# Kernel tuning notes

Measured on AMD Instinct MI355X. Metric: run time of the kernel, lower is better.

Reference implementation:

```python
import jax, jax.numpy as jnp
import numpy as np

QMIN, QMAX = -128.0, 127.0  # int8 range

def setup_inputs() -> dict:
    key = jax.random.key(0)
    k1, k2 = jax.random.split(key)
    B, S, D_IN, D_OUT = 4, 2048, 4096, 4096
    x = jax.random.normal(k1, (B, S, D_IN), dtype=jnp.float32)
    # int8 weight stored as int32 (values in int8 range)
    weight = jax.random.randint(k2, (D_OUT, D_IN), -128, 128, dtype=jnp.int32)
    scale = jnp.array([0.02], dtype=jnp.float32)        # per-tensor weight scale
    input_scale = jnp.array([0.05], dtype=jnp.float32)  # static activation scale
    return {"x": x, "weight": weight, "scale": scale, "input_scale": input_scale}

def reference(x, weight, scale, input_scale):
    # quantize_static_quant_activations: round(x/input_scale) clamped to int8 range,
    # then direct_cast_dequantize back to fp32 (kept as fp32 here; values are integral).
    x_q = jnp.clip(jnp.round(x / input_scale), QMIN, QMAX)
    # direct_cast_dequantize(weight) -> fp32
    w = weight.astype(jnp.float32)
    # F.linear: x_q @ w.T  -> [B, S, D_OUT]
    out = jnp.einsum('bsi,oi->bso', x_q, w)
    # scale_dequantize with combined scale = input_scale * weight_scale
    return out * (input_scale * scale)
```

## Files before the change

kernel.cpp:

```cpp
#include <hip/hip_runtime.h>
#include <stdint.h>

typedef int v4i  __attribute__((ext_vector_type(4)));
typedef int v16i __attribute__((ext_vector_type(16)));

static constexpr int MDIM = 8192;
static constexpr int NDIM = 4096;
static constexpr int KDIM = 4096;

static constexpr int QBLOCKS = (MDIM * KDIM / 16) / 256;
static constexpr int WBLOCKS = (NDIM * KDIM / 16) / 256;

__device__ __forceinline__ void lds_load16(const void* gptr, void* lptr) {
    __builtin_amdgcn_global_load_lds(
        (const __attribute__((address_space(1))) void*)(uintptr_t)gptr,
        (__attribute__((address_space(3))) void*)(uint32_t)(uintptr_t)lptr,
        16, 0, 0);
}

__device__ __forceinline__ int q1(float f, float s) {
    return (int)fminf(fmaxf(__builtin_rintf(f / s), -128.0f), 127.0f);
}
__device__ __forceinline__ int pack4(int a, int b, int c, int d) {
    return (a & 0xff) | ((b & 0xff) << 8) | ((c & 0xff) << 16) | ((d & 0xff) << 24);
}

__global__ __launch_bounds__(256) void prep_k(const float4* __restrict__ x,
                                              int4* __restrict__ xq,
                                              const int4* __restrict__ w,
                                              int4* __restrict__ wq,
                                              const float* __restrict__ s_in) {
    const int b = blockIdx.x;
    if (b < QBLOCKS) {
        const int i = b * 256 + threadIdx.x;
        const float s = s_in[0];
        const float4 v0 = x[4 * i + 0];
        const float4 v1 = x[4 * i + 1];
        const float4 v2 = x[4 * i + 2];
        const float4 v3 = x[4 * i + 3];
        int4 o;
        o.x = pack4(q1(v0.x, s), q1(v0.y, s), q1(v0.z, s), q1(v0.w, s));
        o.y = pack4(q1(v1.x, s), q1(v1.y, s), q1(v1.z, s), q1(v1.w, s));
        o.z = pack4(q1(v2.x, s), q1(v2.y, s), q1(v2.z, s), q1(v2.w, s));
        o.w = pack4(q1(v3.x, s), q1(v3.y, s), q1(v3.z, s), q1(v3.w, s));
        xq[i] = o;
    } else {
        const int i = (b - QBLOCKS) * 256 + threadIdx.x;
        const int4 a = w[4 * i + 0];
        const int4 c = w[4 * i + 1];
        const int4 d = w[4 * i + 2];
        const int4 e = w[4 * i + 3];
        int4 o;
        o.x = pack4(a.x, a.y, a.z, a.w);
        o.y = pack4(c.x, c.y, c.z, c.w);
        o.z = pack4(d.x, d.y, d.z, d.w);
        o.w = pack4(e.x, e.y, e.z, e.w);
        wq[i] = o;
    }
}

__global__ __launch_bounds__(512, 2) void gemm_i8_k(const int8_t* __restrict__ A,
                                                    const int8_t* __restrict__ Bt,
                                                    float* __restrict__ C,
                                                    const float* __restrict__ w_scale,
                                                    const float* __restrict__ in_scale) {
    __shared__ int8_t lds[131072];

    const int tid  = threadIdx.x;
    const int lane = tid & 63;
    const int wave = tid >> 6;
    const int wr = wave >> 2;
    const int wc = wave & 3;
    const int lr = lane & 31;
    const int h  = lane >> 5;

    const int bid = blockIdx.x;
    const int xcd = bid & 7;
    const int j   = bid >> 3;
    const int bm  = (xcd >> 1) * 8 + (j >> 3);
    const int bn  = (xcd & 1) * 8 + (j & 7);

    const int srow  = tid >> 2;
    const int sperm = ((tid & 3) ^ ((tid >> 3) & 3)) << 4;
    const int8_t* gA = A  + (size_t)(bm * 256 + srow) * KDIM + sperm;
    const int8_t* gB = Bt + (size_t)(bn * 256 + srow) * KDIM + sperm;
    const int ldsT = tid * 16;

#define STAGE(MATBASE, GSRC, slot, ks, kbyte)                                              \
    lds_load16(GSRC + (kbyte) + (ks) * 64,                                                 \
               lds + (MATBASE) + (slot) * 32768 + (ks) * 16384 + ldsT);                    \
    lds_load16(GSRC + (kbyte) + (ks) * 64 + 524288,                                        \
               lds + (MATBASE) + (slot) * 32768 + (ks) * 16384 + 8192 + ldsT);

    const int sw0 = ((h ^ ((lr >> 1) & 3)) << 4);
    const int aO0 = (wr * 128 + lr) * 64 + sw0;
    const int aO1 = aO0 ^ 32;
    const int bO0 = 65536 + (wc * 64 + lr) * 64 + sw0;
    const int bO1 = bO0 ^ 32;

    v16i acc[4][2] = {{}};
    v4i a0[4], a1[4], b0[2], b1[2];

#define RD(off) (*(const v4i*)(lds + (off)))
#define VM8 asm volatile("s_waitcnt vmcnt(8)" ::: "memory");
#define VM4 asm volatile("s_waitcnt vmcnt(4)" ::: "memory");
#define VM0 asm volatile("s_waitcnt vmcnt(0)" ::: "memory");

#define SPAN(slot, ks, STA, STB, VMW)                                                      \
    {                                                                                      \
        constexpr int RG = (slot) * 32768 + (ks) * 16384;                                  \
        a0[0] = RD(aO0 + RG + 0 * 2048);                                                   \
        a0[1] = RD(aO0 + RG + 1 * 2048);                                                   \
        a0[2] = RD(aO0 + RG + 2 * 2048);                                                   \
        a0[3] = RD(aO0 + RG + 3 * 2048);                                                   \
        b0[0] = RD(bO0 + RG + 0 * 2048);                                                   \
        b0[1] = RD(bO0 + RG + 1 * 2048);                                                   \
        __builtin_amdgcn_sched_barrier(0);          \
        STA                                                                                \
        a1[0] = RD(aO1 + RG + 0 * 2048);                                                   \
        a1[1] = RD(aO1 + RG + 1 * 2048);                                                   \
        a1[2] = RD(aO1 + RG + 2 * 2048);                                                   \
        a1[3] = RD(aO1 + RG + 3 * 2048);                                                   \
        b1[0] = RD(bO1 + RG + 0 * 2048);                                                   \
        b1[1] = RD(bO1 + RG + 1 * 2048);                                                   \
        STB                                                                                \
        asm volatile("s_waitcnt lgkmcnt(6)" ::: "memory");     \
        __builtin_amdgcn_sched_barrier(0);                                                 \
        __builtin_amdgcn_s_setprio(1);                                                     \
        _Pragma("unroll")                                                                  \
        for (int mt = 0; mt < 4; ++mt)                                                     \
            _Pragma("unroll")                                                              \
            for (int nt = 0; nt < 2; ++nt)                                                 \
                acc[mt][nt] = __builtin_amdgcn_mfma_i32_32x32x32_i8(                       \
                    a0[mt], b0[nt], acc[mt][nt], 0, 0, 0);                                 \
        asm volatile("s_waitcnt lgkmcnt(0)" ::: "memory");   \
        __builtin_amdgcn_sched_barrier(0);                                                 \
        _Pragma("unroll")                                                                  \
        for (int mt = 0; mt < 4; ++mt)                                                     \
            _Pragma("unroll")                                                              \
            for (int nt = 0; nt < 2; ++nt)                                                 \
                acc[mt][nt] = __builtin_amdgcn_mfma_i32_32x32x32_i8(                       \
                    a1[mt], b1[nt], acc[mt][nt], 0, 0, 0);                                 \
        __builtin_amdgcn_s_setprio(0);                                                     \
        VMW                                                                                \
        __builtin_amdgcn_s_barrier();                                                      \
    }

    STAGE(0, gA, 0, 0, 0) STAGE(65536, gB, 0, 0, 0)
    STAGE(0, gA, 0, 1, 0) STAGE(65536, gB, 0, 1, 0)
    STAGE(0, gA, 1, 0, 128) STAGE(65536, gB, 1, 0, 128)
    VM8
    __builtin_amdgcn_s_barrier();

#pragma unroll 1
    for (int it = 0; it < 15; ++it) {
        const int kb = it * 256;
        SPAN(0, 0, STAGE(0, gA, 1, 1, kb + 128), STAGE(65536, gB, 1, 1, kb + 128), VM8)
        SPAN(0, 1, STAGE(0, gA, 0, 0, kb + 256), STAGE(65536, gB, 0, 0, kb + 256), VM8)
        SPAN(1, 0, STAGE(0, gA, 0, 1, kb + 256), STAGE(65536, gB, 0, 1, kb + 256), VM8)
        SPAN(1, 1, STAGE(0, gA, 1, 0, kb + 384), STAGE(65536, gB, 1, 0, kb + 384), VM8)
    }
    SPAN(0, 0, STAGE(0, gA, 1, 1, 3968), STAGE(65536, gB, 1, 1, 3968), VM8)
    SPAN(0, 1, , , VM4)
    SPAN(1, 0, , , VM0)
    SPAN(1, 1, , , )

    const float fs = w_scale[0] * in_scale[0];
    float* Cb = C + (size_t)(bm * 256 + wr * 128 + h * 4) * NDIM + bn * 256 + wc * 64 + lr;
#pragma unroll
    for (int mt = 0; mt < 4; ++mt)
#pragma unroll
        for (int nt = 0; nt < 2; ++nt)
#pragma unroll
            for (int r = 0; r < 16; ++r)
                Cb[(size_t)(mt * 32 + (r & 3) + 8 * (r >> 2)) * NDIM + nt * 32] =
                    (float)acc[mt][nt][r] * fs;

#undef STAGE
#undef RD
#undef SPAN
#undef VM8
#undef VM4
#undef VM0
}

extern "C" void kernel_launch(void* const* d_in, const int* in_sizes, int n_in,
                              void* d_out, int out_size, void* d_ws, size_t ws_size,
                              hipStream_t stream) {
    const float* x        = (const float*)d_in[0];
    const int*   w        = (const int*)d_in[1];
    const float* w_scale  = (const float*)d_in[2];
    const float* in_scale = (const float*)d_in[3];
    float* out = (float*)d_out;

    int8_t* xq = (int8_t*)d_ws;
    int8_t* wq = xq + (size_t)MDIM * KDIM;

    prep_k<<<QBLOCKS + WBLOCKS, 256, 0, stream>>>(
        (const float4*)x, (int4*)xq, (const int4*)w, (int4*)wq, in_scale);

    gemm_i8_k<<<512, 512, 0, stream>>>(xq, wq, out, w_scale, in_scale);
}
```

Before: 406.8 us.

## Prefetch next k-slice LDS fragments across barrier with double-buffered registers

```diff
diff --git a/kernel.cpp b/kernel.cpp
--- a/kernel.cpp
+++ b/kernel.cpp
@@ -74,6 +74,10 @@
     const int lr = lane & 31;
     const int h  = lane >> 5;
 
+    const float fs = w_scale[0] * in_scale[0];
+    asm volatile("s_waitcnt lgkmcnt(0)" ::: "memory");
+    asm volatile("" :: "v"(fs));
+
     const int bid = blockIdx.x;
     const int xcd = bid & 7;
     const int j   = bid >> 3;
@@ -86,86 +90,96 @@
     const int8_t* gB = Bt + (size_t)(bn * 256 + srow) * KDIM + sperm;
     const int ldsT = tid * 16;
 
-#define STAGE(MATBASE, GSRC, slot, ks, kbyte)                                              \
-    lds_load16(GSRC + (kbyte) + (ks) * 64,                                                 \
-               lds + (MATBASE) + (slot) * 32768 + (ks) * 16384 + ldsT);                    \
-    lds_load16(GSRC + (kbyte) + (ks) * 64 + 524288,                                        \
-               lds + (MATBASE) + (slot) * 32768 + (ks) * 16384 + 8192 + ldsT);
-
-    const int sw0 = ((h ^ ((lr >> 1) & 3)) << 4);
-    const int aO0 = (wr * 128 + lr) * 64 + sw0;
-    const int aO1 = aO0 ^ 32;
-    const int bO0 = 65536 + (wc * 64 + lr) * 64 + sw0;
-    const int bO1 = bO0 ^ 32;
+#define RG(slot, ks) ((slot) * 32768 + (ks) * 16384)
+
+#define STG4(slot, ks, kbyte)                                                              \
+    lds_load16(gA + (kbyte) + (ks) * 64,          lds + RG(slot, ks) + ldsT);              \
+    lds_load16(gA + (kbyte) + (ks) * 64 + 524288, lds + RG(slot, ks) + 8192 + ldsT);       \
+    lds_load16(gB + (kbyte) + (ks) * 64,          lds + 65536 + RG(slot, ks) + ldsT);      \
+    lds_load16(gB + (kbyte) + (ks) * 64 + 524288, lds + 65536 + RG(slot, ks) + 8192 + ldsT);
+
+    const int sw  = ((h ^ ((lr >> 1) & 3)) << 4);
+    const int aB0 = (wr * 128 + lr) * 64 + sw;
+    const int aB1 = aB0 ^ 32;
+    const int bB0 = 65536 + (wc * 64 + lr) * 64 + sw;
+    const int bB1 = bB0 ^ 32;
 
     v16i acc[4][2] = {{}};
-    v4i a0[4], a1[4], b0[2], b1[2];
+    v4i av0[2][4], bv0[2][2];
+    v4i av1[4], bv1[2];
 
 #define RD(off) (*(const v4i*)(lds + (off)))
-#define VM8 asm volatile("s_waitcnt vmcnt(8)" ::: "memory");
+
+#define IK0(buf, slot, ks)                                                                 \
+    av0[buf][0] = RD(aB0 + RG(slot, ks) + 0 * 2048);                                       \
+    av0[buf][1] = RD(aB0 + RG(slot, ks) + 1 * 2048);                                       \
+    av0[buf][2] = RD(aB0 + RG(slot, ks) + 2 * 2048);                                       \
+    av0[buf][3] = RD(aB0 + RG(slot, ks) + 3 * 2048);                                       \
+    bv0[buf][0] = RD(bB0 + RG(slot, ks) + 0 * 2048);                                       \
+    bv0[buf][1] = RD(bB0 + RG(slot, ks) + 1 * 2048);
+
+#define IK1(slot, ks)                                                                      \
+    av1[0] = RD(aB1 + RG(slot, ks) + 0 * 2048);                                            \
+    av1[1] = RD(aB1 + RG(slot, ks) + 1 * 2048);                                            \
+    av1[2] = RD(aB1 + RG(slot, ks) + 2 * 2048);                                            \
+    av1[3] = RD(aB1 + RG(slot, ks) + 3 * 2048);                                            \
+    bv1[0] = RD(bB1 + RG(slot, ks) + 0 * 2048);                                            \
+    bv1[1] = RD(bB1 + RG(slot, ks) + 1 * 2048);
+
+#define MFMA8(AARR, BARR)                                                                  \
+    _Pragma("unroll")                                                                      \
+    for (int mt = 0; mt < 4; ++mt)                                                         \
+        _Pragma("unroll")                                                                  \
+        for (int nt = 0; nt < 2; ++nt)                                                     \
+            acc[mt][nt] = __builtin_amdgcn_mfma_i32_32x32x32_i8(                           \
+                AARR[mt], BARR[nt], acc[mt][nt], 0, 0, 0);
+
 #define VM4 asm volatile("s_waitcnt vmcnt(4)" ::: "memory");
 #define VM0 asm volatile("s_waitcnt vmcnt(0)" ::: "memory");
 
-#define SPAN(slot, ks, STA, STB, VMW)                                                      \
+#define PH(CB, IK1S, STG, IKN, G2, VMW)                                                    \
     {                                                                                      \
-        constexpr int RG = (slot) * 32768 + (ks) * 16384;                                  \
-        a0[0] = RD(aO0 + RG + 0 * 2048);                                                   \
-        a0[1] = RD(aO0 + RG + 1 * 2048);                                                   \
-        a0[2] = RD(aO0 + RG + 2 * 2048);                                                   \
-        a0[3] = RD(aO0 + RG + 3 * 2048);                                                   \
-        b0[0] = RD(bO0 + RG + 0 * 2048);                                                   \
-        b0[1] = RD(bO0 + RG + 1 * 2048);                                                   \
-        __builtin_amdgcn_sched_barrier(0);          \
-        STA                                                                                \
-        a1[0] = RD(aO1 + RG + 0 * 2048);                                                   \
-        a1[1] = RD(aO1 + RG + 1 * 2048);                                                   \
-        a1[2] = RD(aO1 + RG + 2 * 2048);                                                   \
-        a1[3] = RD(aO1 + RG + 3 * 2048);                                                   \
-        b1[0] = RD(bO1 + RG + 0 * 2048);                                                   \
-        b1[1] = RD(bO1 + RG + 1 * 2048);                                                   \
-        STB                                                                                \
-        asm volatile("s_waitcnt lgkmcnt(6)" ::: "memory");     \
+        IK1S                                                                               \
+        STG                                                                                \
+        asm volatile("s_waitcnt lgkmcnt(6)" ::: "memory");                                 \
         __builtin_amdgcn_sched_barrier(0);                                                 \
         __builtin_amdgcn_s_setprio(1);                                                     \
-        _Pragma("unroll")                                                                  \
-        for (int mt = 0; mt < 4; ++mt)                                                     \
-            _Pragma("unroll")                                                              \
-            for (int nt = 0; nt < 2; ++nt)                                                 \
-                acc[mt][nt] = __builtin_amdgcn_mfma_i32_32x32x32_i8(                       \
-                    a0[mt], b0[nt], acc[mt][nt], 0, 0, 0);                                 \
-        asm volatile("s_waitcnt lgkmcnt(0)" ::: "memory");   \
-        __builtin_amdgcn_sched_barrier(0);                                                 \
-        _Pragma("unroll")                                                                  \
-        for (int mt = 0; mt < 4; ++mt)                                                     \
-            _Pragma("unroll")                                                              \
-            for (int nt = 0; nt < 2; ++nt)                                                 \
-                acc[mt][nt] = __builtin_amdgcn_mfma_i32_32x32x32_i8(                       \
-                    a1[mt], b1[nt], acc[mt][nt], 0, 0, 0);                                 \
+        MFMA8(av0[CB], bv0[CB])                                                            \
         __builtin_amdgcn_s_setprio(0);                                                     \
+        __builtin_amdgcn_sched_barrier(0);                                                 \
+        IKN                                                                                \
+        asm volatile("s_waitcnt lgkmcnt(" #G2 ")" ::: "memory");                           \
+        __builtin_amdgcn_sched_barrier(0);                                                 \
+        __builtin_amdgcn_s_setprio(1);                                                     \
+        MFMA8(av1, bv1)                                                                    \
+        __builtin_amdgcn_s_setprio(0);                                                     \
+        __builtin_amdgcn_sched_barrier(0);                                                 \
         VMW                                                                                \
         __builtin_amdgcn_s_barrier();                                                      \
+        __builtin_amdgcn_sched_barrier(0);                                                 \
     }
 
-    STAGE(0, gA, 0, 0, 0) STAGE(65536, gB, 0, 0, 0)
-    STAGE(0, gA, 0, 1, 0) STAGE(65536, gB, 0, 1, 0)
-    STAGE(0, gA, 1, 0, 128) STAGE(65536, gB, 1, 0, 128)
-    VM8
+    STG4(0, 0, 0)
+    STG4(0, 1, 0)
+    STG4(1, 0, 128)
+    VM4
     __builtin_amdgcn_s_barrier();
+    __builtin_amdgcn_sched_barrier(0);
+    IK0(0, 0, 0)
 
 #pragma unroll 1
     for (int it = 0; it < 15; ++it) {
         const int kb = it * 256;
-        SPAN(0, 0, STAGE(0, gA, 1, 1, kb + 128), STAGE(65536, gB, 1, 1, kb + 128), VM8)
-        SPAN(0, 1, STAGE(0, gA, 0, 0, kb + 256), STAGE(65536, gB, 0, 0, kb + 256), VM8)
-        SPAN(1, 0, STAGE(0, gA, 0, 1, kb + 256), STAGE(65536, gB, 0, 1, kb + 256), VM8)
-        SPAN(1, 1, STAGE(0, gA, 1, 0, kb + 384), STAGE(65536, gB, 1, 0, kb + 384), VM8)
+        PH(0, IK1(0, 0), STG4(1, 1, kb + 128), IK0(1, 0, 1), 6, VM4)
+        PH(1, IK1(0, 1), STG4(0, 0, kb + 256), IK0(0, 1, 0), 6, VM4)
+        PH(0, IK1(1, 0), STG4(0, 1, kb + 256), IK0(1, 1, 1), 6, VM4)
+        PH(1, IK1(1, 1), STG4(1, 0, kb + 384), IK0(0, 0, 0), 6, VM4)
     }
-    SPAN(0, 0, STAGE(0, gA, 1, 1, 3968), STAGE(65536, gB, 1, 1, 3968), VM8)
-    SPAN(0, 1, , , VM4)
-    SPAN(1, 0, , , VM0)
-    SPAN(1, 1, , , )
-
-    const float fs = w_scale[0] * in_scale[0];
+    PH(0, IK1(0, 0), STG4(1, 1, 3968), IK0(1, 0, 1), 6, VM4)
+    PH(1, IK1(0, 1), ,                 IK0(0, 1, 0), 6, VM0)
+    PH(0, IK1(1, 0), ,                 IK0(1, 1, 1), 6, )
+    PH(1, IK1(1, 1), ,                 ,             0, )
+
     float* Cb = C + (size_t)(bm * 256 + wr * 128 + h * 4) * NDIM + bn * 256 + wc * 64 + lr;
 #pragma unroll
     for (int mt = 0; mt < 4; ++mt)
@@ -176,10 +190,13 @@
                 Cb[(size_t)(mt * 32 + (r & 3) + 8 * (r >> 2)) * NDIM + nt * 32] =
                     (float)acc[mt][nt][r] * fs;
 
-#undef STAGE
+#undef RG
+#undef STG4
 #undef RD
-#undef SPAN
-#undef VM8
+#undef IK0
+#undef IK1
+#undef MFMA8
+#undef PH
 #undef VM4
 #undef VM0
 }
@@ -199,5 +216,6 @@
     prep_k<<<QBLOCKS + WBLOCKS, 256, 0, stream>>>(
         (const float4*)x, (int4*)xq, (const int4*)w, (int4*)wq, in_scale);
 
-    gemm_i8_k<<<512, 512, 0, stream>>>(xq, wq, out, w_scale, in_scale);
-}
+    dim3 grid(512);
+    gemm_i8_k<<<grid, 512, 0, stream>>>(xq, wq, out, w_scale, in_scale);
+}
```

Result: no change. 400.4 us (-1.6%).
